# Kernel tuning notes

Measured on AMD Instinct MI355X. Metric: run time of the kernel, lower is better.

The kernel has to match this reference:

```python
import jax, jax.numpy as jnp
import numpy as np

N = 50000
E = 1600000
IN_DIM = 128
HID = 32
HEADS = 4
OUT = 32
NEG_SLOPE = 0.2


def gat_conv(h, src, dst, W, al, ar, b, n_heads, d_out):
    # h: [N, F_in]; W: [F_in, H*D]; al/ar: [H, D]; b: [H*D]
    n = h.shape[0]
    z = (h @ W).reshape(n, n_heads, d_out)            # [N,H,D]
    el = (z * al[None]).sum(-1)                        # [N,H]
    er = (z * ar[None]).sum(-1)                        # [N,H]
    e = el[src] + er[dst]                              # [E,H]
    e = jnp.where(e > 0, e, NEG_SLOPE * e)             # leaky_relu(0.2)
    # edge softmax grouped by destination node
    m = jax.ops.segment_max(e, dst, num_segments=n)    # [N,H]
    ex = jnp.exp(e - m[dst])                           # [E,H]
    s = jax.ops.segment_sum(ex, dst, num_segments=n)   # [N,H]
    alpha = ex / s[dst]                                # [E,H]
    msg = alpha[:, :, None] * z[src]                   # [E,H,D]
    out = jax.ops.segment_sum(msg, dst, num_segments=n)  # [N,H,D]
    return out + b.reshape(1, n_heads, d_out)


def setup_inputs() -> dict:
    key = jax.random.key(0)
    ks = jax.random.split(key, 12)
    h = jax.random.normal(ks[0], (N, IN_DIM), dtype=jnp.float32)
    src = jax.random.randint(ks[1], (E,), 0, N, dtype=jnp.int32)
    dst = jax.random.randint(ks[2], (E,), 0, N, dtype=jnp.int32)
    s1 = 1.0 / np.sqrt(IN_DIM)
    W1 = jax.random.uniform(ks[3], (IN_DIM, HEADS * HID), jnp.float32, -s1, s1)
    al1 = jax.random.normal(ks[4], (HEADS, HID), jnp.float32) * 0.1
    ar1 = jax.random.normal(ks[5], (HEADS, HID), jnp.float32) * 0.1
    b1 = jnp.zeros((HEADS * HID,), jnp.float32)
    f2 = HEADS * HID
    s2 = 1.0 / np.sqrt(f2)
    W2 = jax.random.uniform(ks[6], (f2, OUT), jnp.float32, -s2, s2)
    al2 = jax.random.normal(ks[7], (1, OUT), jnp.float32) * 0.1
    ar2 = jax.random.normal(ks[8], (1, OUT), jnp.float32) * 0.1
    b2 = jnp.zeros((OUT,), jnp.float32)
    return {"h": h, "src": src, "dst": dst, "W1": W1, "al1": al1, "ar1": ar1,
            "b1": b1, "W2": W2, "al2": al2, "ar2": ar2, "b2": b2}


def reference(h, src, dst, W1, al1, ar1, b1, W2, al2, ar2, b2):
    x = gat_conv(h, src, dst, W1, al1, ar1, b1, HEADS, HID)  # [N,H,D]
    x = x.reshape(N, HEADS * HID)                             # flatten(1)
    x = jax.nn.elu(x)                                         # act
    y = gat_conv(x, src, dst, W2, al2, ar2, b2, 1, OUT)       # [N,1,OUT]
    return y.squeeze(1)                                        # [N,OUT]
```

## Files before the change

kernel.cpp:

```cpp
#include <hip/hip_runtime.h>
#include <hip/hip_fp16.h>

#define NN 50000
#define NEG_SLOPE 0.2f
#define BSHIFT 9
#define BNODES (1 << BSHIFT)
#define NBUCK ((NN + BNODES - 1) >> BSHIFT)
#define BCAP 18432

typedef _Float16 f16x4 __attribute__((ext_vector_type(4)));
typedef _Float16 f16x8 __attribute__((ext_vector_type(8)));
typedef float    f32x4 __attribute__((ext_vector_type(4)));

__global__ void zero_kernel(unsigned* bucket_cursor, int* src_sorted_pad) {
    int i = threadIdx.x;
    if (i < NBUCK) bucket_cursor[i] = (unsigned)(i * BCAP);
    if (i < 64) src_sorted_pad[i] = 0;
}

__global__ __launch_bounds__(1024) void bucketA(
        const int* __restrict__ src, const int* __restrict__ dst,
        unsigned* __restrict__ bucket_cursor, unsigned* __restrict__ ebuf, int E) {
    __shared__ unsigned hist[NBUCK];
    int tid = threadIdx.x;
    if (tid < NBUCK) hist[tid] = 0u;
    __syncthreads();
    int e = blockIdx.x * 1024 + tid;
    int s = 0, d = 0, b = 0;
    bool valid = e < E;
    if (valid) {
        s = src[e]; d = dst[e]; b = d >> BSHIFT;
        atomicAdd(&hist[b], 1u);
    }
    __syncthreads();
    if (tid < NBUCK) {
        unsigned c = hist[tid];
        hist[tid] = c ? atomicAdd(&bucket_cursor[tid], c) : 0u;
    }
    __syncthreads();
    if (valid) {
        unsigned slot = atomicAdd(&hist[b], 1u);
        ebuf[slot] = ((unsigned)s << BSHIFT) | ((unsigned)d & (BNODES - 1));
    }
}

__global__ __launch_bounds__(512) void gemm1_mfma(
        const float* __restrict__ h, const float* __restrict__ W1,
        const float* __restrict__ al1, const float* __restrict__ ar1,
        __half* __restrict__ z1h, float* __restrict__ el1, float* __restrict__ er1, int N) {
    __shared__ alignas(16) __half hA[128 * 128];
    __shared__ alignas(16) __half Bt[128 * 128];
    int tid = threadIdx.x;
    int lane = tid & 63, w = tid >> 6;
    int row0 = blockIdx.x * 128;
    int nrow = min(128, N - row0);

    for (int idx = tid; idx < 128 * 32; idx += 512) {
        int row = idx >> 5, kq = idx & 31;
        float4 v = (row < nrow) ? ((const float4*)(h + (size_t)(row0 + row) * 128))[kq]
                                : make_float4(0.f, 0.f, 0.f, 0.f);
        f16x4 hv;
        hv[0] = (_Float16)v.x; hv[1] = (_Float16)v.y;
        hv[2] = (_Float16)v.z; hv[3] = (_Float16)v.w;
        int off = row * 256 + ((kq * 8) ^ ((row & 15) << 4));
        *(f16x4*)((char*)hA + off) = hv;
    }
    {
        int col = tid & 127, kg = tid >> 7;
        #pragma unroll
        for (int it = 0; it < 4; ++it) {
            int k0 = it * 32 + kg * 8;
            f16x8 wv;
            #pragma unroll
            for (int i = 0; i < 8; ++i)
                wv[i] = (_Float16)W1[(size_t)(k0 + i) * 128 + col];
            int off = col * 256 + ((k0 * 2) ^ ((col & 15) << 4));
            *(f16x8*)((char*)Bt + off) = wv;
        }
    }
    __syncthreads();

    f32x4 acc[8];
    #pragma unroll
    for (int ct = 0; ct < 8; ++ct) acc[ct] = (f32x4){0.f, 0.f, 0.f, 0.f};

    int arow = w * 16 + (lane & 15);
    int kbyte_lane = ((lane >> 4) * 8) * 2;
    #pragma unroll
    for (int ks = 0; ks < 4; ++ks) {
        int kb = ks * 64 + kbyte_lane;
        f16x8 a = *(const f16x8*)((const char*)hA + arow * 256 + (kb ^ ((arow & 15) << 4)));
        #pragma unroll
        for (int ct = 0; ct < 8; ++ct) {
            int col = ct * 16 + (lane & 15);
            f16x8 b = *(const f16x8*)((const char*)Bt + col * 256 + (kb ^ ((col & 15) << 4)));
            acc[ct] = __builtin_amdgcn_mfma_f32_16x16x32_f16(a, b, acc[ct], 0, 0, 0);
        }
    }

    int lrow = (lane >> 4) * 4;
    #pragma unroll
    for (int ct = 0; ct < 8; ++ct) {
        int col = ct * 16 + (lane & 15);
        #pragma unroll
        for (int r = 0; r < 4; ++r) {
            int rl = w * 16 + lrow + r;
            if (rl < nrow)
                z1h[(size_t)(row0 + rl) * 128 + col] = __float2half(acc[ct][r]);
        }
    }
    #pragma unroll
    for (int hh = 0; hh < 4; ++hh) {
        int c0 = hh * 32 + (lane & 15);
        float a_l0 = al1[c0], a_l1 = al1[c0 + 16];
        float a_r0 = ar1[c0], a_r1 = ar1[c0 + 16];
        #pragma unroll
        for (int r = 0; r < 4; ++r) {
            float v0 = acc[2 * hh][r], v1 = acc[2 * hh + 1][r];
            float pl = v0 * a_l0 + v1 * a_l1;
            float pr = v0 * a_r0 + v1 * a_r1;
            #pragma unroll
            for (int o = 8; o; o >>= 1) {
                pl += __shfl_xor(pl, o, 16);
                pr += __shfl_xor(pr, o, 16);
            }
            int rl = w * 16 + lrow + r;
            if ((lane & 15) == 0 && rl < nrow) {
                el1[(row0 + rl) * 4 + hh] = pl;
                er1[(row0 + rl) * 4 + hh] = pr;
            }
        }
    }
}

__global__ __launch_bounds__(1024) void scatterC(
        const unsigned* __restrict__ ebuf, const unsigned* __restrict__ bucket_cursor,
        unsigned* __restrict__ off, int* __restrict__ src_sorted, int N, int E) {
    __shared__ unsigned hist[BNODES], nodeoff[BNODES], wsum[8], bsz[128];
    int b = blockIdx.x, tid = threadIdx.x;
    int base = b << BSHIFT;
    unsigned rs = (unsigned)(b * BCAP), re = bucket_cursor[b];

    if (tid < 128) bsz[tid] = (tid < NBUCK) ? bucket_cursor[tid] - (unsigned)(tid * BCAP) : 0u;
    if (tid < BNODES) hist[tid] = 0u;
    __syncthreads();
    if (tid == 0) {
        unsigned r = 0;
        for (int t = 0; t < NBUCK; ++t) { unsigned c = bsz[t]; bsz[t] = r; r += c; }
        if (b == 0) off[N] = (unsigned)E;
    }
    __syncthreads();
    unsigned boff = bsz[b];

    for (unsigned i = rs + tid; i < re; i += 1024)
        atomicAdd(&hist[ebuf[i] & (BNODES - 1u)], 1u);
    __syncthreads();
    unsigned v = 0, x = 0;
    int lane = tid & 63, wv = tid >> 6;
    if (tid < BNODES) {
        v = hist[tid]; x = v;
        #pragma unroll
        for (int o = 1; o < 64; o <<= 1) {
            unsigned n = __shfl_up(x, o, 64);
            if (lane >= o) x += n;
        }
        if (lane == 63) wsum[wv] = x;
    }
    __syncthreads();
    if (tid == 0) {
        unsigned r = 0;
        #pragma unroll
        for (int k = 0; k < 8; ++k) { unsigned t = wsum[k]; wsum[k] = r; r += t; }
    }
    __syncthreads();
    if (tid < BNODES) {
        unsigned exoff = x - v + wsum[wv] + boff;
        nodeoff[tid] = exoff;
        if (base + tid < N) off[base + tid] = exoff;
        hist[tid] = 0u;
    }
    __syncthreads();
    for (unsigned i = rs + tid; i < re; i += 1024) {
        unsigned pk = ebuf[i];
        unsigned ln = pk & (BNODES - 1u);
        unsigned r = atomicAdd(&hist[ln], 1u);
        src_sorted[nodeoff[ln] + r] = (int)(pk >> BSHIFT);
    }
}

__global__ __launch_bounds__(256) void agg1_spmm(
        const int* __restrict__ src_sorted, const unsigned* __restrict__ off,
        const float* __restrict__ el1, const float* __restrict__ er1,
        const __half* __restrict__ z1h, const float* __restrict__ b1, __half* __restrict__ x) {
    int tid = threadIdx.x, lane = tid & 63, w = tid >> 6;
    int node = blockIdx.x * 4 + w;
    int start = (int)off[node], end = (int)off[node + 1];
    int g = lane >> 4, l16 = lane & 15, head = l16 >> 2;
    const char* zbase = (const char*)z1h + (unsigned)(l16 * 16);
    float er_d = er1[node * 4 + head];

    float acc[8];
    #pragma unroll
    for (int jj = 0; jj < 8; ++jj) acc[jj] = 0.f;
    float sloc = 0.f;
    for (int base = start; base < end; base += 32) {
        #pragma unroll
        for (int t = 0; t < 8; ++t) {
            int i = base + 4 * t + g;
            int s = src_sorted[i];
            float el = el1[(unsigned)s * 4u + head];
            float v = el + er_d;
            v = fmaxf(v, NEG_SLOPE * v);
            float ex = __expf(v);
            ex = (i < end) ? ex : 0.f;
            sloc += ex;
            float4 r = *(const float4*)(zbase + ((unsigned)s << 8));
            const __half* zh = (const __half*)&r;
            #pragma unroll
            for (int k = 0; k < 8; ++k)
                acc[k] = fmaf(__half2float(zh[k]), ex, acc[k]);
        }
    }
    #pragma unroll
    for (int jj = 0; jj < 8; ++jj) {
        acc[jj] += __shfl_xor(acc[jj], 16, 64);
        acc[jj] += __shfl_xor(acc[jj], 32, 64);
    }
    sloc += __shfl_xor(sloc, 16, 64);
    sloc += __shfl_xor(sloc, 32, 64);
    float inv = sloc > 0.f ? 1.f / sloc : 0.f;

    if (g == 0) {
        float xv[8];
        #pragma unroll
        for (int jj = 0; jj < 8; ++jj) {
            float t = acc[jj] * inv + b1[l16 * 8 + jj];
            xv[jj] = t > 0.f ? t : (__expf(t) - 1.f);
        }
        union { __half2 h2[4]; uint4 u; } pk;
        #pragma unroll
        for (int k = 0; k < 4; ++k) pk.h2[k] = __floats2half2_rn(xv[2 * k], xv[2 * k + 1]);
        *(uint4*)(x + ((size_t)node << 7) + l16 * 8) = pk.u;
    }
}

__global__ __launch_bounds__(256) void gemm2el_kernel(
        const __half* __restrict__ x, const float* __restrict__ W2,
        const float* __restrict__ al2, const float* __restrict__ ar2,
        __half* __restrict__ z2h, float* __restrict__ el2, float* __restrict__ er2, int N) {
    __shared__ __half xsh[64][136];
    __shared__ float W2T[32][132];
    int tid = threadIdx.x;
    int row0 = blockIdx.x * 64;
    int nrow = min(64, N - row0);

    for (int idx = tid; idx < nrow * 16; idx += 256) {
        int r = idx >> 4, kq = idx & 15;
        float4 v = ((const float4*)(x + (size_t)(row0 + r) * 128))[kq];
        *(float4*)&xsh[r][kq * 8] = v;
    }
    for (int idx = tid; idx < 4096; idx += 256) {
        int k = idx >> 5, c = idx & 31;
        W2T[c][k] = W2[idx];
    }
    __syncthreads();

    int gc = tid & 15, gr = tid >> 4;
    float acc[4][2];
    #pragma unroll
    for (int j = 0; j < 4; ++j) { acc[j][0] = 0.f; acc[j][1] = 0.f; }

    for (int p = 0; p < 32; ++p) {
        float4 w0 = *(const float4*)&W2T[gc][p * 4];
        float4 w1 = *(const float4*)&W2T[gc + 16][p * 4];
        #pragma unroll
        for (int j = 0; j < 4; ++j) {
            const __half* xr = &xsh[gr * 4 + j][p * 4];
            float x0 = __half2float(xr[0]), x1 = __half2float(xr[1]);
            float x2 = __half2float(xr[2]), x3 = __half2float(xr[3]);
            acc[j][0] = fmaf(x0, w0.x, fmaf(x1, w0.y, fmaf(x2, w0.z, fmaf(x3, w0.w, acc[j][0]))));
            acc[j][1] = fmaf(x0, w1.x, fmaf(x1, w1.y, fmaf(x2, w1.z, fmaf(x3, w1.w, acc[j][1]))));
        }
    }

    float al0 = al2[gc], al1v = al2[gc + 16];
    float ar0 = ar2[gc], ar1v = ar2[gc + 16];
    #pragma unroll
    for (int j = 0; j < 4; ++j) {
        int r = gr * 4 + j;
        int node = row0 + r;
        bool live = r < nrow;
        if (live) {
            z2h[(size_t)node * 32 + gc]      = __float2half(acc[j][0]);
            z2h[(size_t)node * 32 + gc + 16] = __float2half(acc[j][1]);
        }
        float pl = acc[j][0] * al0 + acc[j][1] * al1v;
        float pr = acc[j][0] * ar0 + acc[j][1] * ar1v;
        #pragma unroll
        for (int o = 8; o; o >>= 1) {
            pl += __shfl_xor(pl, o, 16);
            pr += __shfl_xor(pr, o, 16);
        }
        if (live && gc == 0) { el2[node] = pl; er2[node] = pr; }
    }
}

__global__ __launch_bounds__(256) void agg2_fused(
        const int* __restrict__ src_sorted, const unsigned* __restrict__ off,
        const float* __restrict__ el2, const float* __restrict__ er2,
        const __half* __restrict__ z2h, const float* __restrict__ b2,
        float* __restrict__ out) {
    int tid = threadIdx.x, lane = tid & 63;
    int node = blockIdx.x * 4 + (tid >> 6);
    int start = (int)off[node], end = (int)off[node + 1];
    float er_d = er2[node];

    int g = lane >> 2, l4 = lane & 3;
    const char* zbase = (const char*)z2h + (unsigned)(l4 * 16);
    float acc[8];
    #pragma unroll
    for (int jj = 0; jj < 8; ++jj) acc[jj] = 0.f;
    float sloc = 0.f;
    for (int base = start; base < end; base += 64) {
        #pragma unroll
        for (int t = 0; t < 4; ++t) {
            int i = base + 16 * t + g;
            int s = src_sorted[i];
            float v = el2[s] + er_d;
            v = fmaxf(v, NEG_SLOPE * v);
            float ex = __expf(v);
            ex = (i < end) ? ex : 0.f;
            sloc += ex;
            float4 r = *(const float4*)(zbase + ((unsigned)s << 6));
            const __half* zh = (const __half*)&r;
            #pragma unroll
            for (int k = 0; k < 8; ++k)
                acc[k] = fmaf(__half2float(zh[k]), ex, acc[k]);
        }
    }
    #pragma unroll
    for (int jj = 0; jj < 8; ++jj) {
        acc[jj] += __shfl_xor(acc[jj], 4, 64);
        acc[jj] += __shfl_xor(acc[jj], 8, 64);
        acc[jj] += __shfl_xor(acc[jj], 16, 64);
        acc[jj] += __shfl_xor(acc[jj], 32, 64);
    }
    sloc += __shfl_xor(sloc, 4, 64);
    sloc += __shfl_xor(sloc, 8, 64);
    sloc += __shfl_xor(sloc, 16, 64);
    sloc += __shfl_xor(sloc, 32, 64);
    float inv = sloc > 0.f ? 1.f / sloc : 0.f;
    if (g == 0) {
        #pragma unroll
        for (int jj = 0; jj < 8; ++jj)
            out[(size_t)node * 32 + l4 * 8 + jj] = acc[jj] * inv + b2[l4 * 8 + jj];
    }
}

extern "C" void kernel_launch(void* const* d_in, const int* in_sizes, int n_in,
                              void* d_out, int out_size, void* d_ws, size_t ws_size,
                              hipStream_t stream) {
    const float* h   = (const float*)d_in[0];
    const int*   src = (const int*)d_in[1];
    const int*   dst = (const int*)d_in[2];
    const float* W1  = (const float*)d_in[3];
    const float* al1 = (const float*)d_in[4];
    const float* ar1 = (const float*)d_in[5];
    const float* b1  = (const float*)d_in[6];
    const float* W2  = (const float*)d_in[7];
    const float* al2 = (const float*)d_in[8];
    const float* ar2 = (const float*)d_in[9];
    const float* b2  = (const float*)d_in[10];
    float* out = (float*)d_out;
    const int N = NN;
    const int E = in_sizes[1];

    char* w = (char*)d_ws;
    __half* z1h       = (__half*)w;   w += (size_t)N * 128 * 2;
    __half* z2h       = (__half*)w;   w += (size_t)N * 32 * 2;
    __half* xh        = (__half*)w;   w += (size_t)N * 128 * 2;
    unsigned* ebuf    = (unsigned*)w; w += (size_t)NBUCK * BCAP * 4;
    int*   src_sorted = (int*)w;      w += ((size_t)E + 64) * 4;
    float* el1        = (float*)w;    w += (size_t)N * 4 * 4;
    float* er1        = (float*)w;    w += (size_t)N * 4 * 4;
    float* el2        = (float*)w;    w += (size_t)N * 4;
    float* er2        = (float*)w;    w += (size_t)N * 4;
    unsigned* off     = (unsigned*)w; w += (size_t)(N + 16) * 4;
    unsigned* bucket_cursor = (unsigned*)w; w += 128 * 4;

    zero_kernel<<<1, 128, 0, stream>>>(bucket_cursor, src_sorted + E);
    bucketA<<<(E + 1023) / 1024, 1024, 0, stream>>>(src, dst, bucket_cursor, ebuf, E);
    gemm1_mfma<<<(N + 127) / 128, 512, 0, stream>>>(h, W1, al1, ar1, z1h, el1, er1, N);
    scatterC<<<NBUCK, 1024, 0, stream>>>(ebuf, bucket_cursor, off, src_sorted, N, E);
    agg1_spmm<<<N / 4, 256, 0, stream>>>(src_sorted, off, el1, er1, z1h, b1, xh);
    gemm2el_kernel<<<(N + 63) / 64, 256, 0, stream>>>(xh, W2, al2, ar2, z2h, el2, er2, N);
    agg2_fused<<<N / 4, 256, 0, stream>>>(src_sorted, off, el2, er2, z2h, b2, out);
}
```

Baseline: 264.9 us.

## Replace two-pass bucketed CSR build with global atomic histogram, scan, scatter

The old CSR construction binned edges into coarse destination buckets with shared-memory atomics and then ran a per-bucket local sort. It is replaced by a direct global histogram of destinations, a single-block prefix scan, and a scatter that uses a global atomic cursor per node. This drops the intermediate ebuf buffer and the second pass over the edges. In exchange it issues 3.2M global atomics spread over 50k addresses, adds a serial single-block scan over 50k entries, and scatters writes randomly into src_sorted.

```diff
diff --git a/kernel.cpp b/kernel.cpp
--- a/kernel.cpp
+++ b/kernel.cpp
@@ -3,44 +3,64 @@
 
 #define NN 50000
 #define NEG_SLOPE 0.2f
-#define BSHIFT 9
-#define BNODES (1 << BSHIFT)
-#define NBUCK ((NN + BNODES - 1) >> BSHIFT)
-#define BCAP 18432
 
 typedef _Float16 f16x4 __attribute__((ext_vector_type(4)));
 typedef _Float16 f16x8 __attribute__((ext_vector_type(8)));
 typedef float    f32x4 __attribute__((ext_vector_type(4)));
 
-__global__ void zero_kernel(unsigned* bucket_cursor, int* src_sorted_pad) {
-    int i = threadIdx.x;
-    if (i < NBUCK) bucket_cursor[i] = (unsigned)(i * BCAP);
-    if (i < 64) src_sorted_pad[i] = 0;
-}
-
-__global__ __launch_bounds__(1024) void bucketA(
+__global__ void zero2_kernel(unsigned* cnt, int* src_sorted_pad, int N) {
+    int i = blockIdx.x * 256 + threadIdx.x;
+    if (i < N) cnt[i] = 0u;
+    if (blockIdx.x == 0 && threadIdx.x < 64) src_sorted_pad[threadIdx.x] = 0;
+}
+
+__global__ __launch_bounds__(1024) void hist_kernel(
+        const int* __restrict__ dst, unsigned* __restrict__ cnt, int E) {
+    int e = blockIdx.x * 1024 + threadIdx.x;
+    if (e < E) atomicAdd(&cnt[dst[e]], 1u);
+}
+
+__global__ __launch_bounds__(1024) void scan_kernel(
+        const unsigned* __restrict__ cnt, unsigned* __restrict__ off,
+        unsigned* __restrict__ cursor, int N, int E) {
+    __shared__ unsigned wsum[17];
+    int tid = threadIdx.x, lane = tid & 63, wv = tid >> 6;
+    unsigned run = 0;
+    int niter = (N + 1023) / 1024;
+    for (int k = 0; k < niter; ++k) {
+        int i = k * 1024 + tid;
+        unsigned v = (i < N) ? cnt[i] : 0u;
+        unsigned x = v;
+        #pragma unroll
+        for (int o = 1; o < 64; o <<= 1) {
+            unsigned n = __shfl_up(x, o, 64);
+            if (lane >= o) x += n;
+        }
+        if (lane == 63) wsum[wv] = x;
+        __syncthreads();
+        if (tid == 0) {
+            unsigned r = 0;
+            #pragma unroll
+            for (int q = 0; q < 16; ++q) { unsigned t = wsum[q]; wsum[q] = r; r += t; }
+            wsum[16] = r;
+        }
+        __syncthreads();
+        unsigned excl = x - v + wsum[wv] + run;
+        if (i < N) { off[i] = excl; cursor[i] = excl; }
+        run += wsum[16];
+        __syncthreads();
+    }
+    if (tid == 0) off[N] = (unsigned)E;
+}
+
+__global__ __launch_bounds__(1024) void scatter_kernel(
         const int* __restrict__ src, const int* __restrict__ dst,
-        unsigned* __restrict__ bucket_cursor, unsigned* __restrict__ ebuf, int E) {
-    __shared__ unsigned hist[NBUCK];
-    int tid = threadIdx.x;
-    if (tid < NBUCK) hist[tid] = 0u;
-    __syncthreads();
-    int e = blockIdx.x * 1024 + tid;
-    int s = 0, d = 0, b = 0;
-    bool valid = e < E;
-    if (valid) {
-        s = src[e]; d = dst[e]; b = d >> BSHIFT;
-        atomicAdd(&hist[b], 1u);
-    }
-    __syncthreads();
-    if (tid < NBUCK) {
-        unsigned c = hist[tid];
-        hist[tid] = c ? atomicAdd(&bucket_cursor[tid], c) : 0u;
-    }
-    __syncthreads();
-    if (valid) {
-        unsigned slot = atomicAdd(&hist[b], 1u);
-        ebuf[slot] = ((unsigned)s << BSHIFT) | ((unsigned)d & (BNODES - 1));
+        unsigned* __restrict__ cursor, int* __restrict__ src_sorted, int E) {
+    int e = blockIdx.x * 1024 + threadIdx.x;
+    if (e < E) {
+        int d = dst[e], s = src[e];
+        unsigned r = atomicAdd(&cursor[d], 1u);
+        src_sorted[r] = s;
     }
 }
 
@@ -130,61 +150,6 @@
                 er1[(row0 + rl) * 4 + hh] = pr;
             }
         }
-    }
-}
-
-__global__ __launch_bounds__(1024) void scatterC(
-        const unsigned* __restrict__ ebuf, const unsigned* __restrict__ bucket_cursor,
-        unsigned* __restrict__ off, int* __restrict__ src_sorted, int N, int E) {
-    __shared__ unsigned hist[BNODES], nodeoff[BNODES], wsum[8], bsz[128];
-    int b = blockIdx.x, tid = threadIdx.x;
-    int base = b << BSHIFT;
-    unsigned rs = (unsigned)(b * BCAP), re = bucket_cursor[b];
-
-    if (tid < 128) bsz[tid] = (tid < NBUCK) ? bucket_cursor[tid] - (unsigned)(tid * BCAP) : 0u;
-    if (tid < BNODES) hist[tid] = 0u;
-    __syncthreads();
-    if (tid == 0) {
-        unsigned r = 0;
-        for (int t = 0; t < NBUCK; ++t) { unsigned c = bsz[t]; bsz[t] = r; r += c; }
-        if (b == 0) off[N] = (unsigned)E;
-    }
-    __syncthreads();
-    unsigned boff = bsz[b];
-
-    for (unsigned i = rs + tid; i < re; i += 1024)
-        atomicAdd(&hist[ebuf[i] & (BNODES - 1u)], 1u);
-    __syncthreads();
-    unsigned v = 0, x = 0;
-    int lane = tid & 63, wv = tid >> 6;
-    if (tid < BNODES) {
-        v = hist[tid]; x = v;
-        #pragma unroll
-        for (int o = 1; o < 64; o <<= 1) {
-            unsigned n = __shfl_up(x, o, 64);
-            if (lane >= o) x += n;
-        }
-        if (lane == 63) wsum[wv] = x;
-    }
-    __syncthreads();
-    if (tid == 0) {
-        unsigned r = 0;
-        #pragma unroll
-        for (int k = 0; k < 8; ++k) { unsigned t = wsum[k]; wsum[k] = r; r += t; }
-    }
-    __syncthreads();
-    if (tid < BNODES) {
-        unsigned exoff = x - v + wsum[wv] + boff;
-        nodeoff[tid] = exoff;
-        if (base + tid < N) off[base + tid] = exoff;
-        hist[tid] = 0u;
-    }
-    __syncthreads();
-    for (unsigned i = rs + tid; i < re; i += 1024) {
-        unsigned pk = ebuf[i];
-        unsigned ln = pk & (BNODES - 1u);
-        unsigned r = atomicAdd(&hist[ln], 1u);
-        src_sorted[nodeoff[ln] + r] = (int)(pk >> BSHIFT);
     }
 }
 
@@ -379,19 +344,20 @@
     __half* z1h       = (__half*)w;   w += (size_t)N * 128 * 2;
     __half* z2h       = (__half*)w;   w += (size_t)N * 32 * 2;
     __half* xh        = (__half*)w;   w += (size_t)N * 128 * 2;
-    unsigned* ebuf    = (unsigned*)w; w += (size_t)NBUCK * BCAP * 4;
     int*   src_sorted = (int*)w;      w += ((size_t)E + 64) * 4;
     float* el1        = (float*)w;    w += (size_t)N * 4 * 4;
     float* er1        = (float*)w;    w += (size_t)N * 4 * 4;
     float* el2        = (float*)w;    w += (size_t)N * 4;
     float* er2        = (float*)w;    w += (size_t)N * 4;
     unsigned* off     = (unsigned*)w; w += (size_t)(N + 16) * 4;
-    unsigned* bucket_cursor = (unsigned*)w; w += 128 * 4;
-
-    zero_kernel<<<1, 128, 0, stream>>>(bucket_cursor, src_sorted + E);
-    bucketA<<<(E + 1023) / 1024, 1024, 0, stream>>>(src, dst, bucket_cursor, ebuf, E);
+    unsigned* cnt     = (unsigned*)w; w += (size_t)(N + 16) * 4;
+    unsigned* cursor  = (unsigned*)w; w += (size_t)(N + 16) * 4;
+
+    zero2_kernel<<<(N + 255) / 256, 256, 0, stream>>>(cnt, src_sorted + E, N);
+    hist_kernel<<<(E + 1023) / 1024, 1024, 0, stream>>>(dst, cnt, E);
     gemm1_mfma<<<(N + 127) / 128, 512, 0, stream>>>(h, W1, al1, ar1, z1h, el1, er1, N);
-    scatterC<<<NBUCK, 1024, 0, stream>>>(ebuf, bucket_cursor, off, src_sorted, N, E);
+    scan_kernel<<<1, 1024, 0, stream>>>(cnt, off, cursor, N, E);
+    scatter_kernel<<<(E + 1023) / 1024, 1024, 0, stream>>>(src, dst, cursor, src_sorted, E);
     agg1_spmm<<<N / 4, 256, 0, stream>>>(src_sorted, off, el1, er1, z1h, b1, xh);
     gemm2el_kernel<<<(N + 63) / 64, 256, 0, stream>>>(xh, W2, al2, ar2, z2h, el2, er2, N);
     agg2_fused<<<N / 4, 256, 0, stream>>>(src_sorted, off, el2, er2, z2h, b2, out);
```

New measurement: 461.9 us. 74.3% more time.
